# Optimization experiments

Hardware: AMD Instinct MI355X
Metric: run time of the kernel (lower is better)

Reference implementation:

```python
import jax, jax.numpy as jnp
import numpy as np

# Model dims (see init_kwargs)
NU = 4096   # num_users (one-hot feature dim)
NV = 4096   # num_items
C = 5       # num_classes (rating levels)
H0 = 256    # hidden[0]
H1 = 128    # hidden[1]
D_IN = 512  # input_dim (side-feature dense dim)
SIDE = 1024 # raw side-feature dim (u_features.size(1))
NB = 2      # nb basis matrices in bilinear decoder


def setup_inputs() -> dict:
    key = jax.random.key(0)
    ks = jax.random.split(key, 16)
    u = jax.random.randint(ks[0], (4096,), 0, NU)
    v = jax.random.randint(ks[1], (4096,), 0, NV)
    r = jax.random.randint(ks[2], (4096,), 0, C)  # unused by forward (as in source)
    raw = jax.random.randint(ks[3], (NU, NV), 0, 4 * C)
    adj_matrix = (raw[None, :, :] == jnp.arange(1, C + 1)[:, None, None]).astype(jnp.float32)
    u_features = jax.random.normal(ks[4], (NU, SIDE), jnp.float32)
    v_features = jax.random.normal(ks[5], (NV, SIDE), jnp.float32)
    def w(k, shape, fan):
        return jax.random.normal(k, shape, jnp.float32) / np.float32(np.sqrt(fan))
    u_w = w(ks[6], (C, NU, H0), NU)          # per-relation GraphConvolution user weights
    v_w = w(ks[7], (C, NV, H0), NV)          # per-relation item weights
    Wu1 = w(ks[8], (D_IN, SIDE), SIDE); bu1 = jnp.zeros((D_IN,), jnp.float32)
    Wv1 = w(ks[9], (D_IN, SIDE), SIDE); bv1 = jnp.zeros((D_IN,), jnp.float32)
    Wu2 = w(ks[10], (H1, D_IN + H0), D_IN + H0)
    Wv2 = w(ks[11], (H1, D_IN + H0), D_IN + H0)
    P = w(ks[12], (NB, H1, H1), H1)          # bilinear basis matrices
    a = w(ks[13], (NB, C), NB)               # basis -> class coefficients
    return dict(u=u, v=v, r=r, adj_matrix=adj_matrix, u_features=u_features,
                v_features=v_features, u_w=u_w, v_w=v_w, Wu1=Wu1, bu1=bu1,
                Wv1=Wv1, bv1=bv1, Wu2=Wu2, Wv2=Wv2, P=P, a=a)


def reference(u, v, r, adj_matrix, u_features, v_features, u_w, v_w,
              Wu1, bu1, Wv1, bv1, Wu2, Wv2, P, a):
    # m = adj[:, u][:, :, v]  -> [C, nu, nv]
    m = adj_matrix[:, u][:, :, v]
    # degree normalization exactly as written in gc_encoder
    du = jnp.abs(m.sum(axis=1).sum(axis=0))   # [nv]
    di = jnp.abs(m.sum(axis=2).sum(axis=0))   # [nu]
    c = 1.0 / jnp.concatenate([du, di], axis=0)
    c = jnp.where(jnp.isinf(c), jnp.zeros_like(c), c)
    # ordinal weight sharing: W_r = sum_{s<=r} Theta_s; one-hot feat @ W == gather rows
    cu = jnp.cumsum(u_w, axis=0)              # [C, NU, H0]
    cv = jnp.cumsum(v_w, axis=0)
    u_x = cu[:, u]                            # [C, nu, H0]
    v_x = cv[:, v]                            # [C, nv, H0]
    # accumulate per-relation message passing across all C relations at once
    u_next = jnp.einsum('ruv,rvh->uh', m, v_x)   # [nu, H0]
    v_next = jnp.einsum('ruv,ruh->vh', m, u_x)   # [nv, H0]
    z = jax.nn.relu(jnp.concatenate([u_next, v_next], axis=0) * c[:, None])
    nu = u.shape[0]
    u_z, v_z = z[:nu], z[nu:]
    u_f = jax.nn.relu(u_features[u] @ Wu1.T + bu1)
    v_f = jax.nn.relu(v_features[v] @ Wv1.T + bv1)
    u_h = jax.nn.relu(jnp.concatenate([u_z, u_f], axis=1) @ Wu2.T)   # [nu, H1]
    v_h = jax.nn.relu(jnp.concatenate([v_z, v_f], axis=1) @ Wv2.T)   # [nv, H1]
    # bilinear mixture decoder: logits[c,u,v] = sum_b a[b,c] * u_h Q_b v_h^T
    outputs = jnp.einsum('ud,bde,ve,bc->cuv', u_h, P, v_h, a)        # [C, nu, nv]
    logp = jax.nn.log_softmax(outputs, axis=0)
    prob = jnp.exp(logp)
    ratings = jnp.arange(1, C + 1, dtype=outputs.dtype)
    m_hat = jnp.einsum('c,cuv->uv', ratings, prob)
    # losses over observed entries
    mask = m.sum(axis=0) > 0
    n_obs = jnp.maximum(mask.sum(), 1).astype(outputs.dtype)
    loss = -(m * logp).sum() / n_obs
    target = (jnp.argmax(m, axis=0) + 1).astype(outputs.dtype)
    se = jnp.where(mask, (m_hat - target) ** 2, jnp.zeros_like(m_hat))
    rmse_loss = jnp.sqrt(se.sum() / n_obs)
    return (m_hat, loss, rmse_loss)
```

## Files before the change

### kernel.cpp

```cpp
#include <hip/hip_runtime.h>
#include <stdint.h>

#define N4   4096
#define H0   256
#define SIDE 1024
#define DIN  512
#define HCAT 768
#define H1   128
#define NC   5
#define NUV  16777216ULL
#define CAP  1536

typedef __attribute__((ext_vector_type(8))) short short8;
typedef __attribute__((ext_vector_type(4))) float floatx4;

__device__ __forceinline__ unsigned short f2bf(float f) {
    unsigned int u;
    __builtin_memcpy(&u, &f, 4);
    unsigned int r = (u + 0x7FFFu + ((u >> 16) & 1u)) >> 16;
    return (unsigned short)r;
}

__device__ __forceinline__ float bf2f(unsigned short b) {
    unsigned int u = (unsigned int)b << 16;
    float f;
    __builtin_memcpy(&f, &u, 4);
    return f;
}

__global__ __launch_bounds__(256) void k_counts(const int* __restrict__ u,
                                                const int* __restrict__ v,
                                                int* __restrict__ cu,
                                                int* __restrict__ cv) {
    int i = blockIdx.x * 256 + threadIdx.x;
    atomicAdd(&cu[u[i]], 1);
    atomicAdd(&cv[v[i]], 1);
}

__global__ __launch_bounds__(256) void k_code(const float* __restrict__ adj,
                                              uchar4* __restrict__ code4) {
    size_t g = (size_t)blockIdx.x * 256 + threadIdx.x;
    size_t base = g * 4;
    uchar4 out = {0, 0, 0, 0};
    #pragma unroll
    for (int c = 0; c < NC; c++) {
        float4 s = *(const float4*)(adj + (size_t)c * NUV + base);
        out.x = (s.x != 0.f) ? (unsigned char)(c + 1) : out.x;
        out.y = (s.y != 0.f) ? (unsigned char)(c + 1) : out.y;
        out.z = (s.z != 0.f) ? (unsigned char)(c + 1) : out.z;
        out.w = (s.w != 0.f) ? (unsigned char)(c + 1) : out.w;
    }
    code4[g] = out;
}

__global__ __launch_bounds__(256) void k_fuse0(const uint8_t* __restrict__ code,
                                               uint8_t* __restrict__ codeT,
                                               const float* __restrict__ u_w,
                                               const int* __restrict__ cnt_u,
                                               unsigned short* __restrict__ T_Au,
                                               const float* __restrict__ v_w,
                                               const int* __restrict__ cnt_v,
                                               unsigned short* __restrict__ T_Bv) {
    __shared__ __align__(16) uint8_t tile[64][80];
    int b = blockIdx.x, t = threadIdx.x;
    if (b < 4096) {
        int bx = b & 63, by = b >> 6;
        int row = t >> 2;
        int seg = (t & 3) * 16;
        int p0 = by * 64, q0 = bx * 64;
        uint4 vdat = *(const uint4*)(code + (size_t)(p0 + row) * N4 + q0 + seg);
        *(uint4*)(&tile[row][seg]) = vdat;
        __syncthreads();
        union { uint4 u4; uint8_t bb[16]; } o;
        #pragma unroll
        for (int l = 0; l < 16; l++) o.bb[l] = tile[seg + l][row];
        *(uint4*)(codeT + (size_t)(q0 + row) * N4 + p0 + seg) = o.u4;
    } else {
        int node = (b - 4096) & 4095;
        int side = (b - 4096) >> 12;
        const float* w = side ? v_w : u_w;
        const int* cnt = side ? cnt_v : cnt_u;
        unsigned short* out = side ? T_Bv : T_Au;
        int h = t;
        float c = (float)cnt[node];
        float acc = 0.f;
        #pragma unroll
        for (int r = 0; r < NC; r++) {
            size_t idx = ((size_t)r * N4 + node) * H0 + h;
            acc += w[idx];
            union { _Float16 h16; unsigned short s; } cvt;
            cvt.h16 = (_Float16)(acc * c);
            out[idx] = cvt.s;
        }
    }
}

__global__ __launch_bounds__(256) void k_compactF(const uint8_t* __restrict__ code,
                                                  const uint8_t* __restrict__ codeT,
                                                  const int* __restrict__ cnt_u,
                                                  const int* __restrict__ cnt_v,
                                                  unsigned short* __restrict__ idxU,
                                                  int* __restrict__ nnzU,
                                                  float* __restrict__ rowDeg,
                                                  unsigned short* __restrict__ idxV,
                                                  int* __restrict__ nnzV,
                                                  float* __restrict__ colDeg) {
    __shared__ float cw[4096];
    __shared__ int wtot[4];
    __shared__ float wdeg[4];
    __shared__ unsigned short ebuf[CAP];
    int side = blockIdx.y;
    const uint8_t* codeRows = side ? codeT : code;
    const int* cntOther = side ? cnt_u : cnt_v;
    unsigned short* idx = side ? idxV : idxU;
    int* nnz = side ? nnzV : nnzU;
    float* deg = side ? colDeg : rowDeg;

    int p = blockIdx.x, t = threadIdx.x;
    int lane = t & 63, wv = t >> 6;
    const int4* co4 = (const int4*)cntOther;
    #pragma unroll
    for (int l = 0; l < 4; l++) {
        int4 ci = co4[t + l * 256];
        ((float4*)cw)[t + l * 256] =
            make_float4((float)ci.x, (float)ci.y, (float)ci.z, (float)ci.w);
    }
    uint4 w = ((const uint4*)(codeRows + (size_t)p * N4))[t];
    unsigned char b[16];
    __builtin_memcpy(b, &w, 16);
    int cnt = 0;
    #pragma unroll
    for (int j = 0; j < 16; j++) cnt += (b[j] != 0);
    int sc = cnt;
    #pragma unroll
    for (int off = 1; off < 64; off <<= 1) {
        int up = __shfl_up(sc, off, 64);
        if (lane >= off) sc += up;
    }
    if (lane == 63) wtot[wv] = sc;
    __syncthreads();
    int wbase = 0;
    #pragma unroll
    for (int ww = 0; ww < 4; ww++) wbase += (ww < wv) ? wtot[ww] : 0;
    int total = wtot[0] + wtot[1] + wtot[2] + wtot[3];
    int pos = wbase + sc - cnt;
    float dsum = 0.f;
    #pragma unroll
    for (int j = 0; j < 16; j++) {
        int r = b[j];
        if (r) {
            int q = t * 16 + j;
            if (pos < CAP) ebuf[pos] = (unsigned short)((r - 1) * N4 + q);
            pos++;
            dsum += cw[q];
        }
    }
    #pragma unroll
    for (int off = 32; off; off >>= 1) dsum += __shfl_down(dsum, off, 64);
    if (lane == 0) wdeg[wv] = dsum;
    __syncthreads();
    int tw = total < CAP ? total : CAP;
    if (t == 0) { deg[p] = wdeg[0] + wdeg[1] + wdeg[2] + wdeg[3]; nnz[p] = tw; }
    for (int e = t; e < tw; e += 256) idx[(size_t)p * CAP + e] = ebuf[e];
}

__global__ __launch_bounds__(256) void k_gatherF(const unsigned short* __restrict__ idxU,
                                                 const int* __restrict__ nnzU,
                                                 const unsigned short* __restrict__ T_Bv,
                                                 float* __restrict__ u_nn,
                                                 const unsigned short* __restrict__ idxV,
                                                 const int* __restrict__ nnzV,
                                                 const unsigned short* __restrict__ T_Au,
                                                 float* __restrict__ v_nn) {
    __shared__ unsigned short sidx[CAP];
    __shared__ float red[16][132];
    int side = blockIdx.z;
    const unsigned short* idx = side ? idxV : idxU;
    const int* nnz = side ? nnzV : nnzU;
    const char* tb = (const char*)(side ? T_Au : T_Bv);
    float* outNN = side ? v_nn : u_nn;

    int p = blockIdx.x, half = blockIdx.y, t = threadIdx.x;
    int n = nnz[p];
    const unsigned short* rowIdx = idx + (size_t)p * CAP;
    for (int i = t; i < n; i += 256) sidx[i] = rowIdx[i];
    __syncthreads();
    int s = t >> 4;
    int c = t & 15;
    int boff = half * 256 + c * 16;
    float acc[8] = {0.f, 0.f, 0.f, 0.f, 0.f, 0.f, 0.f, 0.f};
    int nmain = n & ~63;
    for (int e = s; e < nmain; e += 64) {
        int o0 = ((int)sidx[e])      << 9;
        int o1 = ((int)sidx[e + 16]) << 9;
        int o2 = ((int)sidx[e + 32]) << 9;
        int o3 = ((int)sidx[e + 48]) << 9;
        uint4 d0 = *(const uint4*)(tb + o0 + boff);
        uint4 d1 = *(const uint4*)(tb + o1 + boff);
        uint4 d2 = *(const uint4*)(tb + o2 + boff);
        uint4 d3 = *(const uint4*)(tb + o3 + boff);
        union { uint4 u; _Float16 h[8]; } cv;
        cv.u = d0;
        #pragma unroll
        for (int k = 0; k < 8; k++) acc[k] += (float)cv.h[k];
        cv.u = d1;
        #pragma unroll
        for (int k = 0; k < 8; k++) acc[k] += (float)cv.h[k];
        cv.u = d2;
        #pragma unroll
        for (int k = 0; k < 8; k++) acc[k] += (float)cv.h[k];
        cv.u = d3;
        #pragma unroll
        for (int k = 0; k < 8; k++) acc[k] += (float)cv.h[k];
    }
    for (int e = nmain + s; e < n; e += 16) {
        int o = ((int)sidx[e]) << 9;
        uint4 d = *(const uint4*)(tb + o + boff);
        union { uint4 u; _Float16 h[8]; } cv;
        cv.u = d;
        #pragma unroll
        for (int k = 0; k < 8; k++) acc[k] += (float)cv.h[k];
    }
    #pragma unroll
    for (int k = 0; k < 8; k++) red[s][c * 8 + k] = acc[k];
    __syncthreads();
    if (t < 128) {
        float sum = 0.f;
        #pragma unroll
        for (int ss = 0; ss < 16; ss++) sum += red[ss][t];
        outNN[(size_t)p * H0 + half * 128 + t] = sum;
    }
}

__global__ __launch_bounds__(256) void k_fuse1(const uint8_t* __restrict__ code,
                                               const int* __restrict__ u,
                                               const int* __restrict__ v,
                                               uint8_t* __restrict__ codeR,
                                               const float* __restrict__ u_nn,
                                               const float* __restrict__ v_nn,
                                               const float* __restrict__ colDeg,
                                               const float* __restrict__ rowDeg,
                                               unsigned short* __restrict__ chiU,
                                               unsigned short* __restrict__ cloU,
                                               unsigned short* __restrict__ chiV,
                                               unsigned short* __restrict__ cloV,
                                               const float* __restrict__ u_feat,
                                               unsigned short* __restrict__ fuhi,
                                               unsigned short* __restrict__ fulo) {
    __shared__ __align__(16) uint8_t rowbuf[4096];
    int b = blockIdx.x, t = threadIdx.x;
    if (b < 4096) {
        int i = b;
        int urow = u[i];
        ((uint4*)rowbuf)[t] = ((const uint4*)(code + (size_t)urow * N4))[t];
        __syncthreads();
        uint8_t ob[16];
        #pragma unroll
        for (int w = 0; w < 4; w++) {
            int4 vv = ((const int4*)v)[t * 4 + w];
            ob[w * 4 + 0] = rowbuf[vv.x];
            ob[w * 4 + 1] = rowbuf[vv.y];
            ob[w * 4 + 2] = rowbuf[vv.z];
            ob[w * 4 + 3] = rowbuf[vv.w];
        }
        uint4 o;
        __builtin_memcpy(&o, ob, 16);
        ((uint4*)(codeR + (size_t)i * N4))[t] = o;
    } else if (b < 12288) {
        int i = (b - 4096) & 4095;
        int side = (b - 4096) >> 12;
        const float* nn = side ? v_nn : u_nn;
        const int* idxs = side ? v : u;
        const int* idxo = side ? u : v;
        const float* deg = side ? rowDeg : colDeg;
        unsigned short* catHi = side ? chiV : chiU;
        unsigned short* catLo = side ? cloV : cloU;
        int h = t;
        float d = deg[idxo[i]];
        float inv = d > 0.f ? 1.f / d : 0.f;
        float val = fmaxf(nn[(size_t)idxs[i] * H0 + h] * inv, 0.f);
        unsigned short hb = f2bf(val);
        catHi[(size_t)i * HCAT + h] = hb;
        catLo[(size_t)i * HCAT + h] = f2bf(val - bf2f(hb));
    } else {
        size_t g = ((size_t)(b - 12288) * 256 + t) * 4;
        float4 x = *(const float4*)(u_feat + g);
        float f[4] = {x.x, x.y, x.z, x.w};
        unsigned short hh[4], ll[4];
        #pragma unroll
        for (int k = 0; k < 4; k++) {
            unsigned short hb = f2bf(f[k]);
            hh[k] = hb;
            ll[k] = f2bf(f[k] - bf2f(hb));
        }
        *(ushort4*)(fuhi + g) = make_ushort4(hh[0], hh[1], hh[2], hh[3]);
        *(ushort4*)(fulo + g) = make_ushort4(ll[0], ll[1], ll[2], ll[3]);
    }
}

__global__ __launch_bounds__(256) void k_fuse2(const float* __restrict__ v_feat,
                                               unsigned short* __restrict__ fvhi,
                                               unsigned short* __restrict__ fvlo,
                                               const float* __restrict__ Wu1,
                                               unsigned short* __restrict__ wuhi,
                                               unsigned short* __restrict__ wulo,
                                               const float* __restrict__ Wv1,
                                               unsigned short* __restrict__ wvhi,
                                               unsigned short* __restrict__ wvlo,
                                               const float* __restrict__ Wu2,
                                               unsigned short* __restrict__ w2uhi,
                                               unsigned short* __restrict__ w2ulo,
                                               const float* __restrict__ Wv2,
                                               unsigned short* __restrict__ w2vhi,
                                               unsigned short* __restrict__ w2vlo,
                                               const float* __restrict__ P,
                                               float* __restrict__ Pt) {
    int b = blockIdx.x, t = threadIdx.x;
    if (b >= 5312) {
        int tid = (b - 5312) * 256 + t;
        int bb = tid >> 14;
        int d = (tid >> 7) & 127;
        int e = tid & 127;
        Pt[((size_t)bb * 128 + e) * 128 + d] = P[tid];
        return;
    }
    const float* src;
    unsigned short* hi;
    unsigned short* lo;
    int lb;
    if (b < 4096)      { src = v_feat; hi = fvhi; lo = fvlo; lb = b; }
    else if (b < 4608) { src = Wu1; hi = wuhi; lo = wulo; lb = b - 4096; }
    else if (b < 5120) { src = Wv1; hi = wvhi; lo = wvlo; lb = b - 4608; }
    else if (b < 5216) { src = Wu2; hi = w2uhi; lo = w2ulo; lb = b - 5120; }
    else               { src = Wv2; hi = w2vhi; lo = w2vlo; lb = b - 5216; }
    size_t g = ((size_t)lb * 256 + t) * 4;
    float4 x = *(const float4*)(src + g);
    float f[4] = {x.x, x.y, x.z, x.w};
    unsigned short hh[4], ll[4];
    #pragma unroll
    for (int k = 0; k < 4; k++) {
        unsigned short hb = f2bf(f[k]);
        hh[k] = hb;
        ll[k] = f2bf(f[k] - bf2f(hb));
    }
    *(ushort4*)(hi + g) = make_ushort4(hh[0], hh[1], hh[2], hh[3]);
    *(ushort4*)(lo + g) = make_ushort4(ll[0], ll[1], ll[2], ll[3]);
}

__global__ __launch_bounds__(256) void k_l1F(const unsigned short* __restrict__ fuhi,
                                             const unsigned short* __restrict__ fulo,
                                             const unsigned short* __restrict__ fvhi,
                                             const unsigned short* __restrict__ fvlo,
                                             const int* __restrict__ u,
                                             const int* __restrict__ v,
                                             const unsigned short* __restrict__ wuhi,
                                             const unsigned short* __restrict__ wulo,
                                             const unsigned short* __restrict__ wvhi,
                                             const unsigned short* __restrict__ wvlo,
                                             const float* __restrict__ bu1,
                                             const float* __restrict__ bv1,
                                             unsigned short* __restrict__ chiU,
                                             unsigned short* __restrict__ cloU,
                                             unsigned short* __restrict__ chiV,
                                             unsigned short* __restrict__ cloV) {
    int side = blockIdx.z;
    const unsigned short* Ahi = side ? fvhi : fuhi;
    const unsigned short* Alo = side ? fvlo : fulo;
    const int* rowmap = side ? v : u;
    const unsigned short* Bhi = side ? wvhi : wuhi;
    const unsigned short* Blo = side ? wvlo : wulo;
    const float* bias = side ? bv1 : bu1;
    unsigned short* CHi = (side ? chiV : chiU) + H0;
    unsigned short* CLo = (side ? cloV : cloU) + H0;

    int t = threadIdx.x;
    int wave = t >> 6, lane = t & 63;
    int lr = lane & 15;
    int lk = lane >> 4;
    int i0 = blockIdx.y * 64 + wave * 16;
    int n0 = blockIdx.x * 64;
    int gi = rowmap[i0 + lr];
    const unsigned short* pah = Ahi + (size_t)gi * SIDE + lk * 8;
    const unsigned short* pal = Alo + (size_t)gi * SIDE + lk * 8;
    floatx4 acc[4];
    #pragma unroll
    for (int jt = 0; jt < 4; jt++) acc[jt] = (floatx4){0.f, 0.f, 0.f, 0.f};
    for (int kc = 0; kc < SIDE / 32; kc++) {
        short8 ah = *(const short8*)(pah + kc * 32);
        short8 al = *(const short8*)(pal + kc * 32);
        #pragma unroll
        for (int jt = 0; jt < 4; jt++) {
            int bc = n0 + jt * 16 + lr;
            short8 bh = *(const short8*)(Bhi + (size_t)bc * SIDE + kc * 32 + lk * 8);
            short8 bl = *(const short8*)(Blo + (size_t)bc * SIDE + kc * 32 + lk * 8);
            acc[jt] = __builtin_amdgcn_mfma_f32_16x16x32_bf16(ah, bh, acc[jt], 0, 0, 0);
            acc[jt] = __builtin_amdgcn_mfma_f32_16x16x32_bf16(ah, bl, acc[jt], 0, 0, 0);
            acc[jt] = __builtin_amdgcn_mfma_f32_16x16x32_bf16(al, bh, acc[jt], 0, 0, 0);
        }
    }
    #pragma unroll
    for (int jt = 0; jt < 4; jt++) {
        int cn = n0 + jt * 16 + lr;
        float b = bias[cn];
        #pragma unroll
        for (int r = 0; r < 4; r++) {
            int ci = i0 + lk * 4 + r;
            float vv = fmaxf(acc[jt][r] + b, 0.f);
            unsigned short hb = f2bf(vv);
            CHi[(size_t)ci * HCAT + cn] = hb;
            CLo[(size_t)ci * HCAT + cn] = f2bf(vv - bf2f(hb));
        }
    }
}

__global__ __launch_bounds__(256) void k_l2F(const unsigned short* __restrict__ chiU,
                                             const unsigned short* __restrict__ cloU,
                                             const unsigned short* __restrict__ w2uhi,
                                             const unsigned short* __restrict__ w2ulo,
                                             float* __restrict__ uh,
                                             const unsigned short* __restrict__ chiV,
                                             const unsigned short* __restrict__ cloV,
                                             const unsigned short* __restrict__ w2vhi,
                                             const unsigned short* __restrict__ w2vlo,
                                             unsigned short* __restrict__ vhb) {
    int side = blockIdx.z;
    const unsigned short* Ahi = side ? chiV : chiU;
    const unsigned short* Alo = side ? cloV : cloU;
    const unsigned short* Bhi = side ? w2vhi : w2uhi;
    const unsigned short* Blo = side ? w2vlo : w2ulo;

    int t = threadIdx.x;
    int wave = t >> 6, lane = t & 63;
    int lr = lane & 15;
    int lk = lane >> 4;
    int i0 = blockIdx.y * 64 + wave * 16;
    int n0 = blockIdx.x * 64;
    const unsigned short* pah = Ahi + (size_t)(i0 + lr) * HCAT + lk * 8;
    const unsigned short* pal = Alo + (size_t)(i0 + lr) * HCAT + lk * 8;
    floatx4 acc[4];
    #pragma unroll
    for (int jt = 0; jt < 4; jt++) acc[jt] = (floatx4){0.f, 0.f, 0.f, 0.f};
    for (int kc = 0; kc < HCAT / 32; kc++) {
        short8 ah = *(const short8*)(pah + kc * 32);
        short8 al = *(const short8*)(pal + kc * 32);
        #pragma unroll
        for (int jt = 0; jt < 4; jt++) {
            int bc = n0 + jt * 16 + lr;
            short8 bh = *(const short8*)(Bhi + (size_t)bc * HCAT + kc * 32 + lk * 8);
            short8 bl = *(const short8*)(Blo + (size_t)bc * HCAT + kc * 32 + lk * 8);
            acc[jt] = __builtin_amdgcn_mfma_f32_16x16x32_bf16(ah, bh, acc[jt], 0, 0, 0);
            acc[jt] = __builtin_amdgcn_mfma_f32_16x16x32_bf16(ah, bl, acc[jt], 0, 0, 0);
            acc[jt] = __builtin_amdgcn_mfma_f32_16x16x32_bf16(al, bh, acc[jt], 0, 0, 0);
        }
    }
    #pragma unroll
    for (int jt = 0; jt < 4; jt++) {
        int cn = n0 + jt * 16 + lr;
        #pragma unroll
        for (int r = 0; r < 4; r++) {
            int ci = i0 + lk * 4 + r;
            float vv = fmaxf(acc[jt][r], 0.f);
            if (side) {
                vhb[(size_t)ci * H1 + cn] = f2bf(vv);
            } else {
                uh[(size_t)ci * H1 + cn] = vv;
            }
        }
    }
}

template <int TM, int TN, int BK, int RM, int RN>
__global__ __launch_bounds__(256) void k_gemm(const float* __restrict__ A, int lda,
                                              const float* __restrict__ B, int ldb,
                                              float* __restrict__ C, int ldc, int K,
                                              size_t bzs, size_t czs) {
    constexpr int TX = TN / RN;
    constexpr int TY = TM / RM;
    static_assert(TX * TY == 256, "block must be 256");
    __shared__ float As[BK][TM + 4];
    __shared__ float Bs[BK][TN + 4];
    int tid = threadIdx.x;
    int tx = tid % TX, ty = tid / TX;
    int i0 = blockIdx.x * TM, n0 = blockIdx.y * TN;
    const float* Bz = B + (size_t)blockIdx.z * bzs;
    float acc[RM][RN] = {};
    for (int k0 = 0; k0 < K; k0 += BK) {
        for (int g = tid; g < TM * BK / 4; g += 256) {
            int i = g / (BK / 4), kc = g % (BK / 4);
            float4 val = *(const float4*)(A + (size_t)(i0 + i) * lda + k0 + kc * 4);
            As[kc * 4 + 0][i] = val.x; As[kc * 4 + 1][i] = val.y;
            As[kc * 4 + 2][i] = val.z; As[kc * 4 + 3][i] = val.w;
        }
        for (int g = tid; g < TN * BK / 4; g += 256) {
            int n = g / (BK / 4), kc = g % (BK / 4);
            float4 val = *(const float4*)(Bz + (size_t)(n0 + n) * ldb + k0 + kc * 4);
            Bs[kc * 4 + 0][n] = val.x; Bs[kc * 4 + 1][n] = val.y;
            Bs[kc * 4 + 2][n] = val.z; Bs[kc * 4 + 3][n] = val.w;
        }
        __syncthreads();
        #pragma unroll
        for (int k = 0; k < BK; k++) {
            float av[RM], bv[RN];
            #pragma unroll
            for (int m = 0; m < RM; m++) av[m] = As[k][ty * RM + m];
            #pragma unroll
            for (int n = 0; n < RN; n++) bv[n] = Bs[k][tx * RN + n];
            #pragma unroll
            for (int m = 0; m < RM; m++)
                #pragma unroll
                for (int n = 0; n < RN; n++)
                    acc[m][n] = fmaf(av[m], bv[n], acc[m][n]);
        }
        __syncthreads();
    }
    #pragma unroll
    for (int m = 0; m < RM; m++) {
        int ig = i0 + ty * RM + m;
        #pragma unroll
        for (int n = 0; n < RN; n++) {
            unsigned short* Cz16 = (unsigned short*)C + (size_t)blockIdx.z * czs;
            Cz16[(size_t)ig * ldc + n0 + tx * RN + n] = f2bf(acc[m][n]);
        }
    }
}

__global__ __launch_bounds__(256) void k_scores3(const unsigned short* __restrict__ tb,
                                                 const unsigned short* __restrict__ vhb,
                                                 const uint8_t* __restrict__ codeR,
                                                 const float* __restrict__ a_f,
                                                 float* __restrict__ mhat,
                                                 float* __restrict__ part) {
    __shared__ float wred[4][3];
    int t = threadIdx.x;
    int wave = t >> 6, lane = t & 63;
    int lr = lane & 15;
    int lk = lane >> 4;
    int i0 = blockIdx.y * 64 + wave * 16;
    int j0 = blockIdx.x * 128;
    float sa0[NC], sa1[NC];
    #pragma unroll
    for (int c = 0; c < NC; c++) { sa0[c] = a_f[c]; sa1[c] = a_f[5 + c]; }

    const unsigned short* t0p = tb;
    const unsigned short* t1p = tb + (size_t)N4 * H1;
    short8 a0[4], a1[4];
    #pragma unroll
    for (int kc = 0; kc < 4; kc++) {
        size_t off = (size_t)(i0 + lr) * H1 + kc * 32 + lk * 8;
        a0[kc] = *(const short8*)(t0p + off);
        a1[kc] = *(const short8*)(t1p + off);
    }

    float lsum = 0.f, ssum = 0.f, nobs = 0.f;
    for (int jt = 0; jt < 8; jt++) {
        int jb = j0 + jt * 16;
        int j = jb + lr;
        const uint8_t* crp = codeR + (size_t)(i0 + lk * 4) * N4 + j;
        int cbv[4];
        cbv[0] = crp[0];
        cbv[1] = crp[N4];
        cbv[2] = crp[2 * N4];
        cbv[3] = crp[3 * N4];
        floatx4 C0 = {0.f, 0.f, 0.f, 0.f}, C1 = {0.f, 0.f, 0.f, 0.f};
        #pragma unroll
        for (int kc = 0; kc < 4; kc++) {
            short8 b = *(const short8*)(vhb + (size_t)(jb + lr) * H1 + kc * 32 + lk * 8);
            C0 = __builtin_amdgcn_mfma_f32_16x16x32_bf16(a0[kc], b, C0, 0, 0, 0);
            C1 = __builtin_amdgcn_mfma_f32_16x16x32_bf16(a1[kc], b, C1, 0, 0, 0);
        }
        #pragma unroll
        for (int r = 0; r < 4; r++) {
            int i = i0 + lk * 4 + r;
            float v0 = C0[r], v1 = C1[r];
            float l[NC];
            float mx = -1e30f;
            #pragma unroll
            for (int c = 0; c < NC; c++) {
                l[c] = sa0[c] * v0 + sa1[c] * v1;
                mx = fmaxf(mx, l[c]);
            }
            float den = 0.f, num = 0.f;
            #pragma unroll
            for (int c = 0; c < NC; c++) {
                float e = __expf(l[c] - mx);
                den += e;
                num += (float)(c + 1) * e;
            }
            float mh = num / den;
            mhat[(size_t)i * N4 + j] = mh;
            int cb = cbv[r];
            if (cb) {
                float lse = mx + __logf(den);
                lsum += lse - l[cb - 1];
                float df = mh - (float)cb;
                ssum += df * df;
                nobs += 1.f;
            }
        }
    }
    #pragma unroll
    for (int off = 32; off; off >>= 1) {
        lsum += __shfl_down(lsum, off, 64);
        ssum += __shfl_down(ssum, off, 64);
        nobs += __shfl_down(nobs, off, 64);
    }
    if (lane == 0) { wred[wave][0] = lsum; wred[wave][1] = ssum; wred[wave][2] = nobs; }
    __syncthreads();
    if (t == 0) {
        int bid = blockIdx.y * gridDim.x + blockIdx.x;
        part[bid * 3 + 0] = wred[0][0] + wred[1][0] + wred[2][0] + wred[3][0];
        part[bid * 3 + 1] = wred[0][1] + wred[1][1] + wred[2][1] + wred[3][1];
        part[bid * 3 + 2] = wred[0][2] + wred[1][2] + wred[2][2] + wred[3][2];
    }
}

__global__ __launch_bounds__(256) void k_finalize(const float* __restrict__ part,
                                                  float* __restrict__ out) {
    __shared__ float sred[3][4];
    int t = threadIdx.x, lane = t & 63, wv = t >> 6;
    float l = 0.f, s = 0.f, n = 0.f;
    for (int i = t; i < 2048; i += 256) {
        l += part[i * 3 + 0];
        s += part[i * 3 + 1];
        n += part[i * 3 + 2];
    }
    #pragma unroll
    for (int off = 32; off; off >>= 1) {
        l += __shfl_down(l, off, 64);
        s += __shfl_down(s, off, 64);
        n += __shfl_down(n, off, 64);
    }
    if (lane == 0) { sred[0][wv] = l; sred[1][wv] = s; sred[2][wv] = n; }
    __syncthreads();
    if (t == 0) {
        float L = sred[0][0] + sred[0][1] + sred[0][2] + sred[0][3];
        float S = sred[1][0] + sred[1][1] + sred[1][2] + sred[1][3];
        float N = fmaxf(sred[2][0] + sred[2][1] + sred[2][2] + sred[2][3], 1.f);
        out[NUV + 0] = L / N;
        out[NUV + 1] = sqrtf(S / N);
    }
}

extern "C" void kernel_launch(void* const* d_in, const int* in_sizes, int n_in,
                              void* d_out, int out_size, void* d_ws, size_t ws_size,
                              hipStream_t stream) {
    const int* u = (const int*)d_in[0];
    const int* v = (const int*)d_in[1];
    const float* adj    = (const float*)d_in[3];
    const float* u_feat = (const float*)d_in[4];
    const float* v_feat = (const float*)d_in[5];
    const float* u_w    = (const float*)d_in[6];
    const float* v_w    = (const float*)d_in[7];
    const float* Wu1    = (const float*)d_in[8];
    const float* bu1    = (const float*)d_in[9];
    const float* Wv1    = (const float*)d_in[10];
    const float* bv1    = (const float*)d_in[11];
    const float* Wu2    = (const float*)d_in[12];
    const float* Wv2    = (const float*)d_in[13];
    const float* P      = (const float*)d_in[14];
    const float* a      = (const float*)d_in[15];
    float* out = (float*)d_out;

    char* ws = (char*)d_ws;
    const size_t O_CODE  = 0;
    const size_t O_CNTU  = 16777216;
    const size_t O_CNTV  = O_CNTU + 16384;
    const size_t O_ACC   = O_CNTV + 16384;
    const size_t O_TAU   = O_ACC + 256;
    const size_t O_TBV   = O_TAU + 10485760;
    const size_t O_IDXU  = O_TBV + 10485760;
    const size_t O_IDXV  = O_IDXU + 12582912;
    const size_t O_NNZU  = O_IDXV + 12582912;
    const size_t O_NNZV  = O_NNZU + 16384;
    const size_t O_RDEG  = O_NNZV + 16384;
    const size_t O_CDEG  = O_RDEG + 16384;
    const size_t O_UNN   = O_CDEG + 16384;
    const size_t O_VNN   = O_UNN + 4194304;
    const size_t O_UCAT  = O_VNN + 4194304;
    const size_t O_VCAT  = O_UCAT + 12582912;
    const size_t O_UH    = O_VCAT + 12582912;
    const size_t O_VHB   = O_UH + 2097152;
    const size_t O_PT    = O_VHB + 1048576;
    const size_t O_TB    = O_PT + 131072;
    const size_t O_CODET = O_UCAT;
    const size_t O_CODER = O_TAU;
    const size_t O_PART  = O_CNTU;
    const size_t O_FUHI  = O_IDXU;
    const size_t O_FULO  = O_IDXV;
    const size_t O_FVHI  = O_CODE;
    const size_t O_FVLO  = O_CODE + 8388608;
    const size_t O_WUHI  = O_UNN;
    const size_t O_WULO  = O_UNN + 1048576;
    const size_t O_WVHI  = O_VNN;
    const size_t O_WVLO  = O_VNN + 1048576;
    const size_t O_CHIU  = O_UCAT;
    const size_t O_CLOU  = O_UCAT + 6291456;
    const size_t O_CHIV  = O_VCAT;
    const size_t O_CLOV  = O_VCAT + 6291456;
    const size_t O_W2UHI = O_TB;
    const size_t O_W2ULO = O_TB + 196608;
    const size_t O_W2VHI = O_TB + 393216;
    const size_t O_W2VLO = O_TB + 589824;

    uint8_t* code  = (uint8_t*)(ws + O_CODE);
    uint8_t* codeT = (uint8_t*)(ws + O_CODET);
    uint8_t* codeR = (uint8_t*)(ws + O_CODER);
    int* cnt_u = (int*)(ws + O_CNTU);
    int* cnt_v = (int*)(ws + O_CNTV);
    unsigned short* T_Au = (unsigned short*)(ws + O_TAU);
    unsigned short* T_Bv = (unsigned short*)(ws + O_TBV);
    unsigned short* idxU = (unsigned short*)(ws + O_IDXU);
    unsigned short* idxV = (unsigned short*)(ws + O_IDXV);
    int* nnzU = (int*)(ws + O_NNZU);
    int* nnzV = (int*)(ws + O_NNZV);
    float* rowDeg = (float*)(ws + O_RDEG);
    float* colDeg = (float*)(ws + O_CDEG);
    float* u_nn = (float*)(ws + O_UNN);
    float* v_nn = (float*)(ws + O_VNN);
    float* uh = (float*)(ws + O_UH);
    unsigned short* vhb = (unsigned short*)(ws + O_VHB);
    float* Pt = (float*)(ws + O_PT);
    unsigned short* tb = (unsigned short*)(ws + O_TB);
    float* part = (float*)(ws + O_PART);
    unsigned short* fuhi = (unsigned short*)(ws + O_FUHI);
    unsigned short* fulo = (unsigned short*)(ws + O_FULO);
    unsigned short* fvhi = (unsigned short*)(ws + O_FVHI);
    unsigned short* fvlo = (unsigned short*)(ws + O_FVLO);
    unsigned short* wuhi = (unsigned short*)(ws + O_WUHI);
    unsigned short* wulo = (unsigned short*)(ws + O_WULO);
    unsigned short* wvhi = (unsigned short*)(ws + O_WVHI);
    unsigned short* wvlo = (unsigned short*)(ws + O_WVLO);
    unsigned short* w2uhi = (unsigned short*)(ws + O_W2UHI);
    unsigned short* w2ulo = (unsigned short*)(ws + O_W2ULO);
    unsigned short* w2vhi = (unsigned short*)(ws + O_W2VHI);
    unsigned short* w2vlo = (unsigned short*)(ws + O_W2VLO);

    hipMemsetAsync(ws + O_CNTU, 0, 16384 + 16384, stream);

    k_counts<<<16, 256, 0, stream>>>(u, v, cnt_u, cnt_v);
    k_code<<<16384, 256, 0, stream>>>(adj, (uchar4*)code);
    k_fuse0<<<12288, 256, 0, stream>>>(code, codeT, u_w, cnt_u, T_Au, v_w, cnt_v, T_Bv);
    k_compactF<<<dim3(N4, 2), 256, 0, stream>>>(code, codeT, cnt_u, cnt_v,
                                                idxU, nnzU, rowDeg, idxV, nnzV, colDeg);
    k_gatherF<<<dim3(N4, 2, 2), 256, 0, stream>>>(idxU, nnzU, T_Bv, u_nn,
                                                  idxV, nnzV, T_Au, v_nn);
    k_fuse1<<<16384, 256, 0, stream>>>(code, u, v, codeR, u_nn, v_nn, colDeg, rowDeg,
                                       (unsigned short*)(ws + O_CHIU), (unsigned short*)(ws + O_CLOU),
                                       (unsigned short*)(ws + O_CHIV), (unsigned short*)(ws + O_CLOV),
                                       u_feat, fuhi, fulo);
    k_fuse2<<<5440, 256, 0, stream>>>(v_feat, fvhi, fvlo, Wu1, wuhi, wulo,
                                      Wv1, wvhi, wvlo, Wu2, w2uhi, w2ulo,
                                      Wv2, w2vhi, w2vlo, P, Pt);
    k_l1F<<<dim3(8, 64, 2), 256, 0, stream>>>(fuhi, fulo, fvhi, fvlo, u, v,
                                              wuhi, wulo, wvhi, wvlo, bu1, bv1,
                                              (unsigned short*)(ws + O_CHIU), (unsigned short*)(ws + O_CLOU),
                                              (unsigned short*)(ws + O_CHIV), (unsigned short*)(ws + O_CLOV));
    k_l2F<<<dim3(2, 64, 2), 256, 0, stream>>>((unsigned short*)(ws + O_CHIU), (unsigned short*)(ws + O_CLOU),
                                              w2uhi, w2ulo, uh,
                                              (unsigned short*)(ws + O_CHIV), (unsigned short*)(ws + O_CLOV),
                                              w2vhi, w2vlo, vhb);
    k_gemm<64, 32, 16, 4, 2>
        <<<dim3(64, 4, 2), 256, 0, stream>>>(uh, H1, Pt, H1,
                                             (float*)tb, H1, H1,
                                             (size_t)H1 * H1, (size_t)N4 * H1);
    k_scores3<<<dim3(32, 64), 256, 0, stream>>>(tb, vhb, codeR, a, out, part);
    k_finalize<<<1, 256, 0, stream>>>(part, out);
}
```

Measured before the change: 1.012 ms.

## Merge launches, stage GEMM B tiles in LDS, prefetch score operands

Folds the count kernel into the code-building kernel and merges the two conversion kernels into one launch, which cuts kernel-launch and tail overhead. Moves the bf16 feature and weight split buffers into the output buffer as scratch, since code and u_nn regions are still live in the merged kernel. The layer-1 and layer-2 GEMMs now stage B tiles in shared memory instead of re-reading them from global per wave. The scores kernel software-pipelines the next vhb and codeR loads. Using the output buffer as scratch depends on it being large enough and on m_hat being written only later.

```diff
diff --git a/kernel.cpp b/kernel.cpp
--- a/kernel.cpp
+++ b/kernel.cpp
@@ -28,29 +28,31 @@
     return f;
 }
 
-__global__ __launch_bounds__(256) void k_counts(const int* __restrict__ u,
-                                                const int* __restrict__ v,
-                                                int* __restrict__ cu,
-                                                int* __restrict__ cv) {
-    int i = blockIdx.x * 256 + threadIdx.x;
-    atomicAdd(&cu[u[i]], 1);
-    atomicAdd(&cv[v[i]], 1);
-}
-
-__global__ __launch_bounds__(256) void k_code(const float* __restrict__ adj,
-                                              uchar4* __restrict__ code4) {
-    size_t g = (size_t)blockIdx.x * 256 + threadIdx.x;
-    size_t base = g * 4;
-    uchar4 out = {0, 0, 0, 0};
-    #pragma unroll
-    for (int c = 0; c < NC; c++) {
-        float4 s = *(const float4*)(adj + (size_t)c * NUV + base);
-        out.x = (s.x != 0.f) ? (unsigned char)(c + 1) : out.x;
-        out.y = (s.y != 0.f) ? (unsigned char)(c + 1) : out.y;
-        out.z = (s.z != 0.f) ? (unsigned char)(c + 1) : out.z;
-        out.w = (s.w != 0.f) ? (unsigned char)(c + 1) : out.w;
-    }
-    code4[g] = out;
+__global__ __launch_bounds__(256) void k_codeF(const float* __restrict__ adj,
+                                               uchar4* __restrict__ code4,
+                                               const int* __restrict__ u,
+                                               const int* __restrict__ v,
+                                               int* __restrict__ cu,
+                                               int* __restrict__ cv) {
+    int b = blockIdx.x, t = threadIdx.x;
+    if (b < 16384) {
+        size_t g = (size_t)b * 256 + t;
+        size_t base = g * 4;
+        uchar4 out = {0, 0, 0, 0};
+        #pragma unroll
+        for (int c = 0; c < NC; c++) {
+            float4 s = *(const float4*)(adj + (size_t)c * NUV + base);
+            out.x = (s.x != 0.f) ? (unsigned char)(c + 1) : out.x;
+            out.y = (s.y != 0.f) ? (unsigned char)(c + 1) : out.y;
+            out.z = (s.z != 0.f) ? (unsigned char)(c + 1) : out.z;
+            out.w = (s.w != 0.f) ? (unsigned char)(c + 1) : out.w;
+        }
+        code4[g] = out;
+    } else {
+        int i = (b - 16384) * 256 + t;
+        atomicAdd(&cu[u[i]], 1);
+        atomicAdd(&cv[v[i]], 1);
+    }
 }
 
 __global__ __launch_bounds__(256) void k_fuse0(const uint8_t* __restrict__ code,
@@ -246,59 +248,8 @@
                                                unsigned short* __restrict__ cloV,
                                                const float* __restrict__ u_feat,
                                                unsigned short* __restrict__ fuhi,
-                                               unsigned short* __restrict__ fulo) {
-    __shared__ __align__(16) uint8_t rowbuf[4096];
-    int b = blockIdx.x, t = threadIdx.x;
-    if (b < 4096) {
-        int i = b;
-        int urow = u[i];
-        ((uint4*)rowbuf)[t] = ((const uint4*)(code + (size_t)urow * N4))[t];
-        __syncthreads();
-        uint8_t ob[16];
-        #pragma unroll
-        for (int w = 0; w < 4; w++) {
-            int4 vv = ((const int4*)v)[t * 4 + w];
-            ob[w * 4 + 0] = rowbuf[vv.x];
-            ob[w * 4 + 1] = rowbuf[vv.y];
-            ob[w * 4 + 2] = rowbuf[vv.z];
-            ob[w * 4 + 3] = rowbuf[vv.w];
-        }
-        uint4 o;
-        __builtin_memcpy(&o, ob, 16);
-        ((uint4*)(codeR + (size_t)i * N4))[t] = o;
-    } else if (b < 12288) {
-        int i = (b - 4096) & 4095;
-        int side = (b - 4096) >> 12;
-        const float* nn = side ? v_nn : u_nn;
-        const int* idxs = side ? v : u;
-        const int* idxo = side ? u : v;
-        const float* deg = side ? rowDeg : colDeg;
-        unsigned short* catHi = side ? chiV : chiU;
-        unsigned short* catLo = side ? cloV : cloU;
-        int h = t;
-        float d = deg[idxo[i]];
-        float inv = d > 0.f ? 1.f / d : 0.f;
-        float val = fmaxf(nn[(size_t)idxs[i] * H0 + h] * inv, 0.f);
-        unsigned short hb = f2bf(val);
-        catHi[(size_t)i * HCAT + h] = hb;
-        catLo[(size_t)i * HCAT + h] = f2bf(val - bf2f(hb));
-    } else {
-        size_t g = ((size_t)(b - 12288) * 256 + t) * 4;
-        float4 x = *(const float4*)(u_feat + g);
-        float f[4] = {x.x, x.y, x.z, x.w};
-        unsigned short hh[4], ll[4];
-        #pragma unroll
-        for (int k = 0; k < 4; k++) {
-            unsigned short hb = f2bf(f[k]);
-            hh[k] = hb;
-            ll[k] = f2bf(f[k] - bf2f(hb));
-        }
-        *(ushort4*)(fuhi + g) = make_ushort4(hh[0], hh[1], hh[2], hh[3]);
-        *(ushort4*)(fulo + g) = make_ushort4(ll[0], ll[1], ll[2], ll[3]);
-    }
-}
-
-__global__ __launch_bounds__(256) void k_fuse2(const float* __restrict__ v_feat,
+                                               unsigned short* __restrict__ fulo,
+                                               const float* __restrict__ v_feat,
                                                unsigned short* __restrict__ fvhi,
                                                unsigned short* __restrict__ fvlo,
                                                const float* __restrict__ Wu1,
@@ -315,9 +266,47 @@
                                                unsigned short* __restrict__ w2vlo,
                                                const float* __restrict__ P,
                                                float* __restrict__ Pt) {
+    __shared__ __align__(16) uint8_t rowbuf[4096];
     int b = blockIdx.x, t = threadIdx.x;
-    if (b >= 5312) {
-        int tid = (b - 5312) * 256 + t;
+    if (b < 4096) {
+        int i = b;
+        int urow = u[i];
+        ((uint4*)rowbuf)[t] = ((const uint4*)(code + (size_t)urow * N4))[t];
+        __syncthreads();
+        uint8_t ob[16];
+        #pragma unroll
+        for (int w = 0; w < 4; w++) {
+            int4 vv = ((const int4*)v)[t * 4 + w];
+            ob[w * 4 + 0] = rowbuf[vv.x];
+            ob[w * 4 + 1] = rowbuf[vv.y];
+            ob[w * 4 + 2] = rowbuf[vv.z];
+            ob[w * 4 + 3] = rowbuf[vv.w];
+        }
+        uint4 o;
+        __builtin_memcpy(&o, ob, 16);
+        ((uint4*)(codeR + (size_t)i * N4))[t] = o;
+        return;
+    }
+    if (b < 12288) {
+        int i = (b - 4096) & 4095;
+        int side = (b - 4096) >> 12;
+        const float* nn = side ? v_nn : u_nn;
+        const int* idxs = side ? v : u;
+        const int* idxo = side ? u : v;
+        const float* deg = side ? rowDeg : colDeg;
+        unsigned short* catHi = side ? chiV : chiU;
+        unsigned short* catLo = side ? cloV : cloU;
+        int h = t;
+        float d = deg[idxo[i]];
+        float inv = d > 0.f ? 1.f / d : 0.f;
+        float val = fmaxf(nn[(size_t)idxs[i] * H0 + h] * inv, 0.f);
+        unsigned short hb = f2bf(val);
+        catHi[(size_t)i * HCAT + h] = hb;
+        catLo[(size_t)i * HCAT + h] = f2bf(val - bf2f(hb));
+        return;
+    }
+    if (b >= 21696) {
+        int tid = (b - 21696) * 256 + t;
         int bb = tid >> 14;
         int d = (tid >> 7) & 127;
         int e = tid & 127;
@@ -328,11 +317,12 @@
     unsigned short* hi;
     unsigned short* lo;
     int lb;
-    if (b < 4096)      { src = v_feat; hi = fvhi; lo = fvlo; lb = b; }
-    else if (b < 4608) { src = Wu1; hi = wuhi; lo = wulo; lb = b - 4096; }
-    else if (b < 5120) { src = Wv1; hi = wvhi; lo = wvlo; lb = b - 4608; }
-    else if (b < 5216) { src = Wu2; hi = w2uhi; lo = w2ulo; lb = b - 5120; }
-    else               { src = Wv2; hi = w2vhi; lo = w2vlo; lb = b - 5216; }
+    if (b < 16384)      { src = u_feat; hi = fuhi; lo = fulo; lb = b - 12288; }
+    else if (b < 20480) { src = v_feat; hi = fvhi; lo = fvlo; lb = b - 16384; }
+    else if (b < 20992) { src = Wu1; hi = wuhi; lo = wulo; lb = b - 20480; }
+    else if (b < 21504) { src = Wv1; hi = wvhi; lo = wvlo; lb = b - 20992; }
+    else if (b < 21600) { src = Wu2; hi = w2uhi; lo = w2ulo; lb = b - 21504; }
+    else                { src = Wv2; hi = w2vhi; lo = w2vlo; lb = b - 21600; }
     size_t g = ((size_t)lb * 256 + t) * 4;
     float4 x = *(const float4*)(src + g);
     float f[4] = {x.x, x.y, x.z, x.w};
@@ -363,6 +353,8 @@
                                              unsigned short* __restrict__ cloU,
                                              unsigned short* __restrict__ chiV,
                                              unsigned short* __restrict__ cloV) {
+    __shared__ unsigned short Bh[64][72];
+    __shared__ unsigned short Bl[64][72];
     int side = blockIdx.z;
     const unsigned short* Ahi = side ? fvhi : fuhi;
     const unsigned short* Alo = side ? fvlo : fulo;
@@ -380,32 +372,44 @@
     int i0 = blockIdx.y * 64 + wave * 16;
     int n0 = blockIdx.x * 64;
     int gi = rowmap[i0 + lr];
-    const unsigned short* pah = Ahi + (size_t)gi * SIDE + lk * 8;
-    const unsigned short* pal = Alo + (size_t)gi * SIDE + lk * 8;
+    const unsigned short* pah = Ahi + (size_t)gi * SIDE;
+    const unsigned short* pal = Alo + (size_t)gi * SIDE;
+    int srow = t >> 2, sseg = (t & 3) * 16;
     floatx4 acc[4];
     #pragma unroll
     for (int jt = 0; jt < 4; jt++) acc[jt] = (floatx4){0.f, 0.f, 0.f, 0.f};
-    for (int kc = 0; kc < SIDE / 32; kc++) {
-        short8 ah = *(const short8*)(pah + kc * 32);
-        short8 al = *(const short8*)(pal + kc * 32);
-        #pragma unroll
-        for (int jt = 0; jt < 4; jt++) {
-            int bc = n0 + jt * 16 + lr;
-            short8 bh = *(const short8*)(Bhi + (size_t)bc * SIDE + kc * 32 + lk * 8);
-            short8 bl = *(const short8*)(Blo + (size_t)bc * SIDE + kc * 32 + lk * 8);
-            acc[jt] = __builtin_amdgcn_mfma_f32_16x16x32_bf16(ah, bh, acc[jt], 0, 0, 0);
-            acc[jt] = __builtin_amdgcn_mfma_f32_16x16x32_bf16(ah, bl, acc[jt], 0, 0, 0);
-            acc[jt] = __builtin_amdgcn_mfma_f32_16x16x32_bf16(al, bh, acc[jt], 0, 0, 0);
+    for (int ks = 0; ks < SIDE / 64; ks++) {
+        const unsigned short* sh = Bhi + (size_t)(n0 + srow) * SIDE + ks * 64 + sseg;
+        const unsigned short* sl = Blo + (size_t)(n0 + srow) * SIDE + ks * 64 + sseg;
+        __syncthreads();
+        *(uint4*)(&Bh[srow][sseg]) = *(const uint4*)sh;
+        *(uint4*)(&Bh[srow][sseg + 8]) = *(const uint4*)(sh + 8);
+        *(uint4*)(&Bl[srow][sseg]) = *(const uint4*)sl;
+        *(uint4*)(&Bl[srow][sseg + 8]) = *(const uint4*)(sl + 8);
+        __syncthreads();
+        #pragma unroll
+        for (int kk = 0; kk < 2; kk++) {
+            int ko = ks * 64 + kk * 32 + lk * 8;
+            short8 ah = *(const short8*)(pah + ko);
+            short8 al = *(const short8*)(pal + ko);
+            #pragma unroll
+            for (int jt = 0; jt < 4; jt++) {
+                short8 bh = *(const short8*)(&Bh[jt * 16 + lr][kk * 32 + lk * 8]);
+                short8 bl = *(const short8*)(&Bl[jt * 16 + lr][kk * 32 + lk * 8]);
+                acc[jt] = __builtin_amdgcn_mfma_f32_16x16x32_bf16(ah, bh, acc[jt], 0, 0, 0);
+                acc[jt] = __builtin_amdgcn_mfma_f32_16x16x32_bf16(ah, bl, acc[jt], 0, 0, 0);
+                acc[jt] = __builtin_amdgcn_mfma_f32_16x16x32_bf16(al, bh, acc[jt], 0, 0, 0);
+            }
         }
     }
     #pragma unroll
     for (int jt = 0; jt < 4; jt++) {
         int cn = n0 + jt * 16 + lr;
-        float b = bias[cn];
+        float bb = bias[cn];
         #pragma unroll
         for (int r = 0; r < 4; r++) {
             int ci = i0 + lk * 4 + r;
-            float vv = fmaxf(acc[jt][r] + b, 0.f);
+            float vv = fmaxf(acc[jt][r] + bb, 0.f);
             unsigned short hb = f2bf(vv);
             CHi[(size_t)ci * HCAT + cn] = hb;
             CLo[(size_t)ci * HCAT + cn] = f2bf(vv - bf2f(hb));
@@ -423,6 +427,8 @@
                                              const unsigned short* __restrict__ w2vhi,
                                              const unsigned short* __restrict__ w2vlo,
                                              unsigned short* __restrict__ vhb) {
+    __shared__ unsigned short Bh[64][72];
+    __shared__ unsigned short Bl[64][72];
     int side = blockIdx.z;
     const unsigned short* Ahi = side ? chiV : chiU;
     const unsigned short* Alo = side ? cloV : cloU;
@@ -435,22 +441,34 @@
     int lk = lane >> 4;
     int i0 = blockIdx.y * 64 + wave * 16;
     int n0 = blockIdx.x * 64;
-    const unsigned short* pah = Ahi + (size_t)(i0 + lr) * HCAT + lk * 8;
-    const unsigned short* pal = Alo + (size_t)(i0 + lr) * HCAT + lk * 8;
+    const unsigned short* pah = Ahi + (size_t)(i0 + lr) * HCAT;
+    const unsigned short* pal = Alo + (size_t)(i0 + lr) * HCAT;
+    int srow = t >> 2, sseg = (t & 3) * 16;
     floatx4 acc[4];
     #pragma unroll
     for (int jt = 0; jt < 4; jt++) acc[jt] = (floatx4){0.f, 0.f, 0.f, 0.f};
-    for (int kc = 0; kc < HCAT / 32; kc++) {
-        short8 ah = *(const short8*)(pah + kc * 32);
-        short8 al = *(const short8*)(pal + kc * 32);
-        #pragma unroll
-        for (int jt = 0; jt < 4; jt++) {
-            int bc = n0 + jt * 16 + lr;
-            short8 bh = *(const short8*)(Bhi + (size_t)bc * HCAT + kc * 32 + lk * 8);
-            short8 bl = *(const short8*)(Blo + (size_t)bc * HCAT + kc * 32 + lk * 8);
-            acc[jt] = __builtin_amdgcn_mfma_f32_16x16x32_bf16(ah, bh, acc[jt], 0, 0, 0);
-            acc[jt] = __builtin_amdgcn_mfma_f32_16x16x32_bf16(ah, bl, acc[jt], 0, 0, 0);
-            acc[jt] = __builtin_amdgcn_mfma_f32_16x16x32_bf16(al, bh, acc[jt], 0, 0, 0);
+    for (int ks = 0; ks < HCAT / 64; ks++) {
+        const unsigned short* sh = Bhi + (size_t)(n0 + srow) * HCAT + ks * 64 + sseg;
+        const unsigned short* sl = Blo + (size_t)(n0 + srow) * HCAT + ks * 64 + sseg;
+        __syncthreads();
+        *(uint4*)(&Bh[srow][sseg]) = *(const uint4*)sh;
+        *(uint4*)(&Bh[srow][sseg + 8]) = *(const uint4*)(sh + 8);
+        *(uint4*)(&Bl[srow][sseg]) = *(const uint4*)sl;
+        *(uint4*)(&Bl[srow][sseg + 8]) = *(const uint4*)(sl + 8);
+        __syncthreads();
+        #pragma unroll
+        for (int kk = 0; kk < 2; kk++) {
+            int ko = ks * 64 + kk * 32 + lk * 8;
+            short8 ah = *(const short8*)(pah + ko);
+            short8 al = *(const short8*)(pal + ko);
+            #pragma unroll
+            for (int jt = 0; jt < 4; jt++) {
+                short8 bh = *(const short8*)(&Bh[jt * 16 + lr][kk * 32 + lk * 8]);
+                short8 bl = *(const short8*)(&Bl[jt * 16 + lr][kk * 32 + lk * 8]);
+                acc[jt] = __builtin_amdgcn_mfma_f32_16x16x32_bf16(ah, bh, acc[jt], 0, 0, 0);
+                acc[jt] = __builtin_amdgcn_mfma_f32_16x16x32_bf16(ah, bl, acc[jt], 0, 0, 0);
+                acc[jt] = __builtin_amdgcn_mfma_f32_16x16x32_bf16(al, bh, acc[jt], 0, 0, 0);
+            }
         }
     }
     #pragma unroll
@@ -551,22 +569,43 @@
         a1[kc] = *(const short8*)(t1p + off);
     }
 
+    const uint8_t* crbase = codeR + (size_t)(i0 + lk * 4) * N4 + lr;
+    short8 bcur[4];
+    int cbv[4];
+    {
+        int jb = j0;
+        const uint8_t* crp = crbase + jb;
+        cbv[0] = crp[0];
+        cbv[1] = crp[N4];
+        cbv[2] = crp[2 * N4];
+        cbv[3] = crp[3 * N4];
+        #pragma unroll
+        for (int kc = 0; kc < 4; kc++)
+            bcur[kc] = *(const short8*)(vhb + (size_t)(jb + lr) * H1 + kc * 32 + lk * 8);
+    }
+
     float lsum = 0.f, ssum = 0.f, nobs = 0.f;
     for (int jt = 0; jt < 8; jt++) {
         int jb = j0 + jt * 16;
         int j = jb + lr;
-        const uint8_t* crp = codeR + (size_t)(i0 + lk * 4) * N4 + j;
-        int cbv[4];
-        cbv[0] = crp[0];
-        cbv[1] = crp[N4];
-        cbv[2] = crp[2 * N4];
-        cbv[3] = crp[3 * N4];
+        short8 bnext[4];
+        int cbn[4];
+        if (jt < 7) {
+            int jb2 = jb + 16;
+            const uint8_t* crp = crbase + jb2;
+            cbn[0] = crp[0];
+            cbn[1] = crp[N4];
+            cbn[2] = crp[2 * N4];
+            cbn[3] = crp[3 * N4];
+            #pragma unroll
+            for (int kc = 0; kc < 4; kc++)
+                bnext[kc] = *(const short8*)(vhb + (size_t)(jb2 + lr) * H1 + kc * 32 + lk * 8);
+        }
         floatx4 C0 = {0.f, 0.f, 0.f, 0.f}, C1 = {0.f, 0.f, 0.f, 0.f};
         #pragma unroll
         for (int kc = 0; kc < 4; kc++) {
-            short8 b = *(const short8*)(vhb + (size_t)(jb + lr) * H1 + kc * 32 + lk * 8);
-            C0 = __builtin_amdgcn_mfma_f32_16x16x32_bf16(a0[kc], b, C0, 0, 0, 0);
-            C1 = __builtin_amdgcn_mfma_f32_16x16x32_bf16(a1[kc], b, C1, 0, 0, 0);
+            C0 = __builtin_amdgcn_mfma_f32_16x16x32_bf16(a0[kc], bcur[kc], C0, 0, 0, 0);
+            C1 = __builtin_amdgcn_mfma_f32_16x16x32_bf16(a1[kc], bcur[kc], C1, 0, 0, 0);
         }
         #pragma unroll
         for (int r = 0; r < 4; r++) {
@@ -596,6 +635,12 @@
                 ssum += df * df;
                 nobs += 1.f;
             }
+        }
+        if (jt < 7) {
+            #pragma unroll
+            for (int kc = 0; kc < 4; kc++) bcur[kc] = bnext[kc];
+            #pragma unroll
+            for (int r = 0; r < 4; r++) cbv[r] = cbn[r];
         }
     }
     #pragma unroll
@@ -687,20 +732,20 @@
     const size_t O_PART  = O_CNTU;
     const size_t O_FUHI  = O_IDXU;
     const size_t O_FULO  = O_IDXV;
-    const size_t O_FVHI  = O_CODE;
-    const size_t O_FVLO  = O_CODE + 8388608;
-    const size_t O_WUHI  = O_UNN;
-    const size_t O_WULO  = O_UNN + 1048576;
-    const size_t O_WVHI  = O_VNN;
-    const size_t O_WVLO  = O_VNN + 1048576;
     const size_t O_CHIU  = O_UCAT;
     const size_t O_CLOU  = O_UCAT + 6291456;
     const size_t O_CHIV  = O_VCAT;
     const size_t O_CLOV  = O_VCAT + 6291456;
-    const size_t O_W2UHI = O_TB;
-    const size_t O_W2ULO = O_TB + 196608;
-    const size_t O_W2VHI = O_TB + 393216;
-    const size_t O_W2VLO = O_TB + 589824;
+    const size_t S_FVHI  = 0;
+    const size_t S_FVLO  = 8388608;
+    const size_t S_WUHI  = 16777216;
+    const size_t S_WULO  = S_WUHI + 1048576;
+    const size_t S_WVHI  = S_WULO + 1048576;
+    const size_t S_WVLO  = S_WVHI + 1048576;
+    const size_t S_W2UHI = S_WVLO + 1048576;
+    const size_t S_W2ULO = S_W2UHI + 196608;
+    const size_t S_W2VHI = S_W2ULO + 196608;
+    const size_t S_W2VLO = S_W2VHI + 196608;
 
     uint8_t* code  = (uint8_t*)(ws + O_CODE);
     uint8_t* codeT = (uint8_t*)(ws + O_CODET);
@@ -724,41 +769,42 @@
     float* part = (float*)(ws + O_PART);
     unsigned short* fuhi = (unsigned short*)(ws + O_FUHI);
     unsigned short* fulo = (unsigned short*)(ws + O_FULO);
-    unsigned short* fvhi = (unsigned short*)(ws + O_FVHI);
-    unsigned short* fvlo = (unsigned short*)(ws + O_FVLO);
-    unsigned short* wuhi = (unsigned short*)(ws + O_WUHI);
-    unsigned short* wulo = (unsigned short*)(ws + O_WULO);
-    unsigned short* wvhi = (unsigned short*)(ws + O_WVHI);
-    unsigned short* wvlo = (unsigned short*)(ws + O_WVLO);
-    unsigned short* w2uhi = (unsigned short*)(ws + O_W2UHI);
-    unsigned short* w2ulo = (unsigned short*)(ws + O_W2ULO);
-    unsigned short* w2vhi = (unsigned short*)(ws + O_W2VHI);
-    unsigned short* w2vlo = (unsigned short*)(ws + O_W2VLO);
+    unsigned short* chiU = (unsigned short*)(ws + O_CHIU);
+    unsigned short* cloU = (unsigned short*)(ws + O_CLOU);
+    unsigned short* chiV = (unsigned short*)(ws + O_CHIV);
+    unsigned short* cloV = (unsigned short*)(ws + O_CLOV);
+    char* outc = (char*)d_out;
+    unsigned short* fvhi = (unsigned short*)(outc + S_FVHI);
+    unsigned short* fvlo = (unsigned short*)(outc + S_FVLO);
+    unsigned short* wuhi = (unsigned short*)(outc + S_WUHI);
+    unsigned short* wulo = (unsigned short*)(outc + S_WULO);
+    unsigned short* wvhi = (unsigned short*)(outc + S_WVHI);
+    unsigned short* wvlo = (unsigned short*)(outc + S_WVLO);
+    unsigned short* w2uhi = (unsigned short*)(outc + S_W2UHI);
+    unsigned short* w2ulo = (unsigned short*)(outc + S_W2ULO);
+    unsigned short* w2vhi = (unsigned short*)(outc + S_W2VHI);
+    unsigned short* w2vlo = (unsigned short*)(outc + S_W2VLO);
 
     hipMemsetAsync(ws + O_CNTU, 0, 16384 + 16384, stream);
 
-    k_counts<<<16, 256, 0, stream>>>(u, v, cnt_u, cnt_v);
-    k_code<<<16384, 256, 0, stream>>>(adj, (uchar4*)code);
+    k_codeF<<<16400, 256, 0, stream>>>(adj, (uchar4*)code, u, v, cnt_u, cnt_v);
     k_fuse0<<<12288, 256, 0, stream>>>(code, codeT, u_w, cnt_u, T_Au, v_w, cnt_v, T_Bv);
     k_compactF<<<dim3(N4, 2), 256, 0, stream>>>(code, codeT, cnt_u, cnt_v,
                                                 idxU, nnzU, rowDeg, idxV, nnzV, colDeg);
     k_gatherF<<<dim3(N4, 2, 2), 256, 0, stream>>>(idxU, nnzU, T_Bv, u_nn,
                                                   idxV, nnzV, T_Au, v_nn);
-    k_fuse1<<<16384, 256, 0, stream>>>(code, u, v, codeR, u_nn, v_nn, colDeg, rowDeg,
-                                       (unsigned short*)(ws + O_CHIU), (unsigned short*)(ws + O_CLOU),
-                                       (unsigned short*)(ws + O_CHIV), (unsigned short*)(ws + O_CLOV),
-                                       u_feat, fuhi, fulo);
-    k_fuse2<<<5440, 256, 0, stream>>>(v_feat, fvhi, fvlo, Wu1, wuhi, wulo,
-                                      Wv1, wvhi, wvlo, Wu2, w2uhi, w2ulo,
-                                      Wv2, w2vhi, w2vlo, P, Pt);
+    k_fuse1<<<21824, 256, 0, stream>>>(code, u, v, codeR, u_nn, v_nn, colDeg, rowDeg,
+                                       chiU, cloU, chiV, cloV,
+                                       u_feat, fuhi, fulo,
+                                       v_feat, fvhi, fvlo,
+                                       Wu1, wuhi, wulo, Wv1, wvhi, wvlo,
+                                       Wu2, w2uhi, w2ulo, Wv2, w2vhi, w2vlo,
+                                       P, Pt);
     k_l1F<<<dim3(8, 64, 2), 256, 0, stream>>>(fuhi, fulo, fvhi, fvlo, u, v,
                                               wuhi, wulo, wvhi, wvlo, bu1, bv1,
-                                              (unsigned short*)(ws + O_CHIU), (unsigned short*)(ws + O_CLOU),
-                                              (unsigned short*)(ws + O_CHIV), (unsigned short*)(ws + O_CLOV));
-    k_l2F<<<dim3(2, 64, 2), 256, 0, stream>>>((unsigned short*)(ws + O_CHIU), (unsigned short*)(ws + O_CLOU),
-                                              w2uhi, w2ulo, uh,
-                                              (unsigned short*)(ws + O_CHIV), (unsigned short*)(ws + O_CLOV),
-                                              w2vhi, w2vlo, vhb);
+                                              chiU, cloU, chiV, cloV);
+    k_l2F<<<dim3(2, 64, 2), 256, 0, stream>>>(chiU, cloU, w2uhi, w2ulo, uh,
+                                              chiV, cloV, w2vhi, w2vlo, vhb);
     k_gemm<64, 32, 16, 4, 2>
         <<<dim3(64, 4, 2), 256, 0, stream>>>(uh, H1, Pt, H1,
                                              (float*)tb, H1, H1,
```

Result: faster. 891.8 us (-11.9%).
